# Performance work log

Measured on AMD Instinct MI355X. Metric: run time of the kernel, lower is better.

Reference implementation:

```python
import jax, jax.numpy as jnp
import numpy as np

HIDDEN = 128

def setup_inputs() -> dict:
    key = jax.random.key(0)
    ks = jax.random.split(key, 7)
    B, T, H = 1024, 512, HIDDEN
    x = jax.random.normal(ks[0], (B, T, 1), dtype=jnp.float32)
    # xavier_normal for W_ih [H, 1]: std = sqrt(2/(fan_in+fan_out)) = sqrt(2/(1+H))
    W_ih = jax.random.normal(ks[1], (H, 1), dtype=jnp.float32) * np.sqrt(2.0 / (1 + H))
    # orthogonal init for W_hh [H, H]
    A = jax.random.normal(ks[2], (H, H), dtype=jnp.float32)
    Q, _ = jnp.linalg.qr(A)
    W_hh = Q.astype(jnp.float32)
    bound = 1.0 / np.sqrt(H)
    b_ih = jax.random.uniform(ks[3], (H,), minval=-bound, maxval=bound, dtype=jnp.float32)
    b_hh = jax.random.uniform(ks[4], (H,), minval=-bound, maxval=bound, dtype=jnp.float32)
    W_out = jax.random.uniform(ks[5], (1, H), minval=-bound, maxval=bound, dtype=jnp.float32)
    b_out = jax.random.uniform(ks[6], (1,), minval=-bound, maxval=bound, dtype=jnp.float32)
    return {"x": x, "W_ih": W_ih, "W_hh": W_hh, "b_ih": b_ih, "b_hh": b_hh, "W_out": W_out, "b_out": b_out}

def reference(x, W_ih, W_hh, b_ih, b_hh, W_out, b_out):
    B, T, _ = x.shape
    H = W_hh.shape[0]
    # Precompute input projection for all timesteps: [T, B, H]
    xp = jnp.einsum('bti,hi->tbh', x, W_ih) + (b_ih + b_hh)
    h0 = jnp.zeros((B, H), dtype=x.dtype)

    def step(h, xp_t):
        h_new = jnp.tanh(xp_t + h @ W_hh.T)
        return h_new, None

    h_last, _ = jax.lax.scan(step, h0, xp)
    y = h_last @ W_out.T + b_out  # [B, 1]
    return y
```

## Files before the change

### kernel.cpp

```cpp
#include <hip/hip_runtime.h>

#define T_STEPS 512
#define HID 128
#define ROWS 16
#define SCALE 2.885390081777926816f

typedef short bf16x8 __attribute__((ext_vector_type(8)));
typedef float f32x4  __attribute__((ext_vector_type(4)));
typedef unsigned int u32;
typedef u32 u32x4 __attribute__((ext_vector_type(4)));


#define XW_OFF   8192
#define Z_OFF    73728
#define RED_OFF  73744
#define LDS_BYTES (73744 + 512)

__device__ __forceinline__ u32 cvt_pk_bf16(float s0, float s1) {
    u32 d;
    asm("v_cvt_pk_bf16_f32 %0, %1, %2" : "=v"(d) : "v"(s0), "v"(s1));
    return d;
}
__device__ __forceinline__ bf16x8 frag_from(u32 a, u32 b, u32 c, u32 d) {
    u32x4 t = {a, b, c, d};
    return __builtin_bit_cast(bf16x8, t);
}

#define MFMA(ACC, A, B) \
    ACC = __builtin_amdgcn_mfma_f32_16x16x32_bf16(A, B, ACC, 0, 0, 0);

__global__ __launch_bounds__(512, 1)
__attribute__((amdgpu_waves_per_eu(2, 2)))
void rnn_lean5_kernel(const float* __restrict__ x,
                      const float* __restrict__ W_ih,
                      const float* __restrict__ W_hh,
                      const float* __restrict__ b_ih,
                      const float* __restrict__ b_hh,
                      const float* __restrict__ W_out,
                      const float* __restrict__ b_out,
                      float* __restrict__ y)
{
    __shared__ __align__(16) char lds[LDS_BYTES];

    const int tid = threadIdx.x;
    const int w   = tid >> 6;
    const int l   = tid & 63;
    const int q   = l >> 4;
    const int r   = l & 15;
    const int b0  = blockIdx.x * ROWS;

    *(uint2*)&lds[tid * 8] = make_uint2(0u, 0u);
    if (tid == 0) *(uint2*)&lds[Z_OFF] = make_uint2(0u, 0u);

    for (int i = tid; i < ROWS * T_STEPS; i += 512) {
        const int rr = i >> 9;
        const int tt = i & 511;
        const float xv = x[(size_t)(b0 + rr) * T_STEPS + tt];
        const u32 w0 = cvt_pk_bf16(1.0f, xv);
        const float xh = __uint_as_float(w0 & 0xffff0000u);
        const u32 w1 = cvt_pk_bf16(xh, xv - xh);
        *(uint2*)&lds[XW_OFF + (tt * 16 + rr) * 8] = make_uint2(w0, w1);
    }

    bf16x8 WH0, WH1, WH2, WH3;
    {
        const float* p = W_hh + (size_t)(16 * w + r) * HID + 8 * q;
#define LDW(DST, OFF) do {                                                    \
    float4 fa_ = *(const float4*)(p + (OFF));                                 \
    float4 fb_ = *(const float4*)(p + (OFF) + 4);                             \
    DST = frag_from(cvt_pk_bf16(fa_.x*SCALE, fa_.y*SCALE),                    \
                    cvt_pk_bf16(fa_.z*SCALE, fa_.w*SCALE),                    \
                    cvt_pk_bf16(fb_.x*SCALE, fb_.y*SCALE),                    \
                    cvt_pk_bf16(fb_.z*SCALE, fb_.w*SCALE));                   \
} while (0)
        LDW(WH0,  0); LDW(WH1, 32); LDW(WH2, 64); LDW(WH3, 96);
#undef LDW
    }

    bf16x8 Ap;
    {
        const int jA = 16 * w + r;
        const float bias = (b_ih[jA] + b_hh[jA]) * SCALE;
        const float wih  = W_ih[jA] * SCALE;
        const float bm   = (q == 0) ? bias : 0.0f;
        const float wm   = (q == 0) ? wih  : 0.0f;
        const u32 w0 = cvt_pk_bf16(bm, wm);
        const float wl = wm - __uint_as_float(w0 & 0xffff0000u);
        const float bl = bm - __uint_as_float(w0 << 16);
        const u32 w1 = cvt_pk_bf16(wl, wm);
        const u32 w2 = cvt_pk_bf16(bl, 0.0f);
        Ap = frag_from(w0, w1, w2, 0u);
    }
    const u32 bpw2 = cvt_pk_bf16((q == 0) ? 1.0f : 0.0f, 0.0f);

    const int j0 = 16 * w + 4 * q;

    const int rswz  = ((r >> 3) << 4) ^ ((q & 1) << 5);
    const int roff0 = ((l * 16) ^ rswz);
    const int cw    = j0 >> 5;
    const int qw    = (j0 >> 3) & 3;
    const int woff  = cw * 1024 +
        ((((qw * 16 + r) * 16) + (j0 & 7) * 2) ^ ((r >> 3) << 4) ^ ((qw & 1) << 5));

    u32 xaddr        = (q == 0) ? (u32)(XW_OFF + r * 8) : (u32)Z_OFF;
    const u32 xstride = (q == 0) ? 128u : 0u;

    f32x4 hv;
    __syncthreads();

#define STEP(RB, WB) do {                                                     \
    const bf16x8 B0 = *(const bf16x8*)&lds[(RB) + roff0];                     \
    const bf16x8 B1 = *(const bf16x8*)&lds[(RB) + roff0 + 1024];              \
    const bf16x8 B2 = *(const bf16x8*)&lds[(RB) + roff0 + 2048];              \
    const bf16x8 B3 = *(const bf16x8*)&lds[(RB) + roff0 + 3072];              \
    const uint2 bw  = *(const uint2*)&lds[xaddr];                             \
    const bf16x8 Bp = frag_from(bw.x, bw.y, bpw2, 0u);                        \
    f32x4 acc = __builtin_amdgcn_mfma_f32_16x16x32_bf16(                      \
        Ap, Bp, (f32x4)(0.0f), 0, 0, 0);                                      \
    MFMA(acc, WH0, B0) MFMA(acc, WH1, B1)                                     \
    MFMA(acc, WH2, B2) MFMA(acc, WH3, B3)                                     \
    const float e0 = __builtin_amdgcn_exp2f(acc[0]);                          \
    const float e1 = __builtin_amdgcn_exp2f(acc[1]);                          \
    const float e2 = __builtin_amdgcn_exp2f(acc[2]);                          \
    const float e3 = __builtin_amdgcn_exp2f(acc[3]);                          \
    const float rc0 = __builtin_amdgcn_rcpf(e0 + 1.0f);                       \
    const float rc1 = __builtin_amdgcn_rcpf(e1 + 1.0f);                       \
    const float rc2 = __builtin_amdgcn_rcpf(e2 + 1.0f);                       \
    const float rc3 = __builtin_amdgcn_rcpf(e3 + 1.0f);                       \
    hv[0] = fmaf(-2.0f, rc0, 1.0f); hv[1] = fmaf(-2.0f, rc1, 1.0f);           \
    hv[2] = fmaf(-2.0f, rc2, 1.0f); hv[3] = fmaf(-2.0f, rc3, 1.0f);           \
    *(uint2*)&lds[(WB) + woff] =                                              \
        make_uint2(cvt_pk_bf16(hv[0], hv[1]), cvt_pk_bf16(hv[2], hv[3]));     \
    xaddr += xstride;                                                         \
    __syncthreads();                                                          \
} while (0)

    for (int t = 0; t < T_STEPS; t += 2) {
        STEP(0,    4096);
        STEP(4096, 0);
    }
#undef STEP

    const float4 wo = *(const float4*)(W_out + j0);
    float v = wo.x*hv[0] + wo.y*hv[1] + wo.z*hv[2] + wo.w*hv[3];
    v += __shfl_xor(v, 16, 64);
    v += __shfl_xor(v, 32, 64);
    if (l < 16) *(float*)&lds[RED_OFF + (w * 16 + r) * 4] = v;
    __syncthreads();
    if (tid < 16) {
        float s = 0.0f;
        #pragma unroll
        for (int ww = 0; ww < 8; ++ww)
            s += *(const float*)&lds[RED_OFF + (ww * 16 + tid) * 4];
        y[b0 + tid] = s + b_out[0];
    }
}

extern "C" void kernel_launch(void* const* d_in, const int* in_sizes, int n_in,
                              void* d_out, int out_size, void* d_ws, size_t ws_size,
                              hipStream_t stream)
{
    const float* x     = (const float*)d_in[0];
    const float* W_ih  = (const float*)d_in[1];
    const float* W_hh  = (const float*)d_in[2];
    const float* b_ih  = (const float*)d_in[3];
    const float* b_hh  = (const float*)d_in[4];
    const float* W_out = (const float*)d_in[5];
    const float* b_out = (const float*)d_in[6];
    float* y = (float*)d_out;

    const int B = in_sizes[0] / T_STEPS;
    rnn_lean5_kernel<<<B / ROWS, 512, 0, stream>>>(x, W_ih, W_hh, b_ih, b_hh,
                                                   W_out, b_out, y);
}
```

Measured before the change: 134.7 us.

## Process two independent 16-row batch groups per 1024-thread block

Each block now holds two independent sequence groups of 16 rows, with 16 waves sharing one block-wide barrier per timestep. Each group gets its own h double-buffer and x staging area in LDS. This halves the block count to 32 and raises resident waves per CU to 4, so the MFMA and transcendental latency of one group can overlap with the other's. The costs are LDS use growing to about 148 KB per block and every barrier now synchronising twice as many waves.

```diff
diff --git a/kernel.cpp b/kernel.cpp
--- a/kernel.cpp
+++ b/kernel.cpp
@@ -3,6 +3,7 @@
 #define T_STEPS 512
 #define HID 128
 #define ROWS 16
+#define SEQS 2
 #define SCALE 2.885390081777926816f
 
 typedef short bf16x8 __attribute__((ext_vector_type(8)));
@@ -11,10 +12,11 @@
 typedef u32 u32x4 __attribute__((ext_vector_type(4)));
 
 
-#define XW_OFF   8192
-#define Z_OFF    73728
-#define RED_OFF  73744
-#define LDS_BYTES (73744 + 512)
+#define HB(S)    ((S) * 8192)
+#define XW(S)    (16384 + (S) * 65536)
+#define Z_OFF    147456
+#define RED_OFF  147472
+#define LDS_BYTES (147472 + 1024)
 
 __device__ __forceinline__ u32 cvt_pk_bf16(float s0, float s1) {
     u32 d;
@@ -29,42 +31,46 @@
 #define MFMA(ACC, A, B) \
     ACC = __builtin_amdgcn_mfma_f32_16x16x32_bf16(A, B, ACC, 0, 0, 0);
 
-__global__ __launch_bounds__(512, 1)
-__attribute__((amdgpu_waves_per_eu(2, 2)))
-void rnn_lean5_kernel(const float* __restrict__ x,
-                      const float* __restrict__ W_ih,
-                      const float* __restrict__ W_hh,
-                      const float* __restrict__ b_ih,
-                      const float* __restrict__ b_hh,
-                      const float* __restrict__ W_out,
-                      const float* __restrict__ b_out,
-                      float* __restrict__ y)
+__global__ __launch_bounds__(1024)
+__attribute__((amdgpu_waves_per_eu(4, 4)))
+void rnn_lean_x2_kernel(const float* __restrict__ x,
+                        const float* __restrict__ W_ih,
+                        const float* __restrict__ W_hh,
+                        const float* __restrict__ b_ih,
+                        const float* __restrict__ b_hh,
+                        const float* __restrict__ W_out,
+                        const float* __restrict__ b_out,
+                        float* __restrict__ y)
 {
     __shared__ __align__(16) char lds[LDS_BYTES];
 
     const int tid = threadIdx.x;
     const int w   = tid >> 6;
+    const int s   = w >> 3;
+    const int wv  = w & 7;
     const int l   = tid & 63;
     const int q   = l >> 4;
     const int r   = l & 15;
-    const int b0  = blockIdx.x * ROWS;
+    const int b0  = blockIdx.x * (SEQS * ROWS);
 
-    *(uint2*)&lds[tid * 8] = make_uint2(0u, 0u);
+    *(uint2*)&lds[(tid >> 9) * 8192 + (tid & 511) * 8] = make_uint2(0u, 0u);
     if (tid == 0) *(uint2*)&lds[Z_OFF] = make_uint2(0u, 0u);
 
-    for (int i = tid; i < ROWS * T_STEPS; i += 512) {
-        const int rr = i >> 9;
-        const int tt = i & 511;
-        const float xv = x[(size_t)(b0 + rr) * T_STEPS + tt];
+    for (int i = tid; i < SEQS * ROWS * T_STEPS; i += 1024) {
+        const int s_  = i >> 13;
+        const int rem = i & 8191;
+        const int rr  = rem >> 9;
+        const int tt  = rem & 511;
+        const float xv = x[(size_t)(b0 + s_ * ROWS + rr) * T_STEPS + tt];
         const u32 w0 = cvt_pk_bf16(1.0f, xv);
         const float xh = __uint_as_float(w0 & 0xffff0000u);
         const u32 w1 = cvt_pk_bf16(xh, xv - xh);
-        *(uint2*)&lds[XW_OFF + (tt * 16 + rr) * 8] = make_uint2(w0, w1);
+        *(uint2*)&lds[XW(s_) + (tt * 16 + rr) * 8] = make_uint2(w0, w1);
     }
 
     bf16x8 WH0, WH1, WH2, WH3;
     {
-        const float* p = W_hh + (size_t)(16 * w + r) * HID + 8 * q;
+        const float* p = W_hh + (size_t)(16 * wv + r) * HID + 8 * q;
 #define LDW(DST, OFF) do {                                                    \
     float4 fa_ = *(const float4*)(p + (OFF));                                 \
     float4 fb_ = *(const float4*)(p + (OFF) + 4);                             \
@@ -79,7 +85,7 @@
 
     bf16x8 Ap;
     {
-        const int jA = 16 * w + r;
+        const int jA = 16 * wv + r;
         const float bias = (b_ih[jA] + b_hh[jA]) * SCALE;
         const float wih  = W_ih[jA] * SCALE;
         const float bm   = (q == 0) ? bias : 0.0f;
@@ -93,7 +99,7 @@
     }
     const u32 bpw2 = cvt_pk_bf16((q == 0) ? 1.0f : 0.0f, 0.0f);
 
-    const int j0 = 16 * w + 4 * q;
+    const int j0 = 16 * wv + 4 * q;
 
     const int rswz  = ((r >> 3) << 4) ^ ((q & 1) << 5);
     const int roff0 = ((l * 16) ^ rswz);
@@ -102,17 +108,18 @@
     const int woff  = cw * 1024 +
         ((((qw * 16 + r) * 16) + (j0 & 7) * 2) ^ ((r >> 3) << 4) ^ ((qw & 1) << 5));
 
-    u32 xaddr        = (q == 0) ? (u32)(XW_OFF + r * 8) : (u32)Z_OFF;
+    u32 xaddr         = (q == 0) ? (u32)(XW(s) + r * 8) : (u32)Z_OFF;
     const u32 xstride = (q == 0) ? 128u : 0u;
 
+    const u32 hb = (u32)HB(s);
     f32x4 hv;
     __syncthreads();
 
 #define STEP(RB, WB) do {                                                     \
-    const bf16x8 B0 = *(const bf16x8*)&lds[(RB) + roff0];                     \
-    const bf16x8 B1 = *(const bf16x8*)&lds[(RB) + roff0 + 1024];              \
-    const bf16x8 B2 = *(const bf16x8*)&lds[(RB) + roff0 + 2048];              \
-    const bf16x8 B3 = *(const bf16x8*)&lds[(RB) + roff0 + 3072];              \
+    const bf16x8 B0 = *(const bf16x8*)&lds[hb + (RB) + roff0];                \
+    const bf16x8 B1 = *(const bf16x8*)&lds[hb + (RB) + roff0 + 1024];         \
+    const bf16x8 B2 = *(const bf16x8*)&lds[hb + (RB) + roff0 + 2048];         \
+    const bf16x8 B3 = *(const bf16x8*)&lds[hb + (RB) + roff0 + 3072];         \
     const uint2 bw  = *(const uint2*)&lds[xaddr];                             \
     const bf16x8 Bp = frag_from(bw.x, bw.y, bpw2, 0u);                        \
     f32x4 acc = __builtin_amdgcn_mfma_f32_16x16x32_bf16(                      \
@@ -129,7 +136,7 @@
     const float rc3 = __builtin_amdgcn_rcpf(e3 + 1.0f);                       \
     hv[0] = fmaf(-2.0f, rc0, 1.0f); hv[1] = fmaf(-2.0f, rc1, 1.0f);           \
     hv[2] = fmaf(-2.0f, rc2, 1.0f); hv[3] = fmaf(-2.0f, rc3, 1.0f);           \
-    *(uint2*)&lds[(WB) + woff] =                                              \
+    *(uint2*)&lds[hb + (WB) + woff] =                                         \
         make_uint2(cvt_pk_bf16(hv[0], hv[1]), cvt_pk_bf16(hv[2], hv[3]));     \
     xaddr += xstride;                                                         \
     __syncthreads();                                                          \
@@ -145,14 +152,15 @@
     float v = wo.x*hv[0] + wo.y*hv[1] + wo.z*hv[2] + wo.w*hv[3];
     v += __shfl_xor(v, 16, 64);
     v += __shfl_xor(v, 32, 64);
-    if (l < 16) *(float*)&lds[RED_OFF + (w * 16 + r) * 4] = v;
+    if (l < 16) *(float*)&lds[RED_OFF + s * 512 + (wv * 16 + r) * 4] = v;
     __syncthreads();
-    if (tid < 16) {
-        float s = 0.0f;
+    if (tid < 32) {
+        const int ss = tid >> 4, rr = tid & 15;
+        float acc = 0.0f;
         #pragma unroll
         for (int ww = 0; ww < 8; ++ww)
-            s += *(const float*)&lds[RED_OFF + (ww * 16 + tid) * 4];
-        y[b0 + tid] = s + b_out[0];
+            acc += *(const float*)&lds[RED_OFF + ss * 512 + (ww * 16 + rr) * 4];
+        y[b0 + ss * ROWS + rr] = acc + b_out[0];
     }
 }
 
@@ -170,6 +178,6 @@
     float* y = (float*)d_out;
 
     const int B = in_sizes[0] / T_STEPS;
-    rnn_lean5_kernel<<<B / ROWS, 512, 0, stream>>>(x, W_ih, W_hh, b_ih, b_hh,
-                                                   W_out, b_out, y);
+    rnn_lean_x2_kernel<<<B / (SEQS * ROWS), 1024, 0, stream>>>(
+        x, W_ih, W_hh, b_ih, b_hh, W_out, b_out, y);
 }
```

After: 198.7 us. 1.48x slower.
